# Optimization experiments

Hardware: AMD Instinct MI355X
Metric: run time of the kernel (lower is better)

## Reference

```python
import jax, jax.numpy as jnp
import numpy as np

B, S, H, L, V, T = 128, 512, 512, 2, 30, 64  # batch, enc len, hidden, layers, vocab, decode len


def _p(k, shape):
    return jax.random.normal(k, shape, jnp.float32) * 0.05


def setup_inputs() -> dict:
    key = jax.random.key(0)
    ks = jax.random.split(key, 24)
    inp = {"x": jax.random.normal(ks[0], (B, S, 2), jnp.float32)}
    inp["emb"] = _p(ks[1], (V, H))
    # encoder GRU (input dim 2 for layer 0, H for layer 1); PyTorch gate order r,z,n
    inp["enc_Wih0"] = _p(ks[2], (3 * H, 2));  inp["enc_Whh0"] = _p(ks[3], (3 * H, H))
    inp["enc_bih0"] = _p(ks[4], (3 * H,));    inp["enc_bhh0"] = _p(ks[5], (3 * H,))
    inp["enc_Wih1"] = _p(ks[6], (3 * H, H));  inp["enc_Whh1"] = _p(ks[7], (3 * H, H))
    inp["enc_bih1"] = _p(ks[8], (3 * H,));    inp["enc_bhh1"] = _p(ks[9], (3 * H,))
    # decoder GRU (input dim H)
    inp["dec_Wih0"] = _p(ks[10], (3 * H, H)); inp["dec_Whh0"] = _p(ks[11], (3 * H, H))
    inp["dec_bih0"] = _p(ks[12], (3 * H,));   inp["dec_bhh0"] = _p(ks[13], (3 * H,))
    inp["dec_Wih1"] = _p(ks[14], (3 * H, H)); inp["dec_Whh1"] = _p(ks[15], (3 * H, H))
    inp["dec_bih1"] = _p(ks[16], (3 * H,));   inp["dec_bhh1"] = _p(ks[17], (3 * H,))
    inp["fc_W"] = _p(ks[18], (V, 2 * H));     inp["fc_b"] = _p(ks[19], (V,))
    return inp


def gru_cell(xt, h, Wih, Whh, bih, bhh):
    gi = xt @ Wih.T + bih
    gh = h @ Whh.T + bhh
    i_r, i_z, i_n = jnp.split(gi, 3, axis=-1)
    h_r, h_z, h_n = jnp.split(gh, 3, axis=-1)
    r = jax.nn.sigmoid(i_r + h_r)
    z = jax.nn.sigmoid(i_z + h_z)
    n = jnp.tanh(i_n + r * h_n)
    return (1.0 - z) * n + z * h


def _forward(x, emb,
             enc_Wih0, enc_Whh0, enc_bih0, enc_bhh0,
             enc_Wih1, enc_Whh1, enc_bih1, enc_bhh1,
             dec_Wih0, dec_Whh0, dec_bih0, dec_bhh0,
             dec_Wih1, dec_Whh1, dec_bih1, dec_bhh1,
             fc_W, fc_b):
    b = x.shape[0]
    h0 = jnp.zeros((b, H), x.dtype)

    # ---- encoder: 2-layer GRU scanned over time ----
    def enc_step(hs, xt):
        a = gru_cell(xt, hs[0], enc_Wih0, enc_Whh0, enc_bih0, enc_bhh0)
        c = gru_cell(a, hs[1], enc_Wih1, enc_Whh1, enc_bih1, enc_bhh1)
        return (a, c), c

    (e0, e1), out_enc_t = jax.lax.scan(enc_step, (h0, h0), x.transpose(1, 0, 2))
    out_enc = out_enc_t.transpose(1, 0, 2)  # [B, S, H]

    def dec_step(carry, _):
        (d0, d1), tok = carry
        e = emb[tok]  # [B, H]
        n0 = gru_cell(e, d0, dec_Wih0, dec_Whh0, dec_bih0, dec_bhh0)
        n1 = gru_cell(n0, d1, dec_Wih1, dec_Whh1, dec_bih1, dec_bhh1)
        out_dec = n1  # [B, H]
        sim = jnp.einsum('bsh,bh->bs', out_enc, out_dec)  # [B, S]
        # faithful to nn.Softmax() implicit dim on 3-D [B,S,1] tensor -> dim=0 (batch)
        att_w = jax.nn.softmax(sim, axis=0)
        attention = jnp.einsum('bs,bsh->bh', att_w, out_enc)  # [B, H]
        logits = jnp.concatenate([out_dec, attention], axis=-1) @ fc_W.T + fc_b  # [B, V]
        tok_next = jnp.argmax(logits, axis=-1)
        return ((n0, n1), tok_next), logits

    tok0 = jnp.zeros((b,), jnp.int32)
    ((f0, f1), _), logits_t = jax.lax.scan(dec_step, ((e0, e1), tok0), None, length=T)
    vec_out = logits_t.transpose(1, 0, 2)  # [B, T, V]
    hidden = jnp.stack([f0, f1], axis=0)   # [n_layers, B, H]
    return vec_out, hidden


def reference(x, emb,
              enc_Wih0, enc_Whh0, enc_bih0, enc_bhh0,
              enc_Wih1, enc_Whh1, enc_bih1, enc_bhh1,
              dec_Wih0, dec_Whh0, dec_bih0, dec_bhh0,
              dec_Wih1, dec_Whh1, dec_bih1, dec_bhh1,
              fc_W, fc_b):
    return _forward(x, emb,
                    enc_Wih0, enc_Whh0, enc_bih0, enc_bhh0,
                    enc_Wih1, enc_Whh1, enc_bih1, enc_bhh1,
                    dec_Wih0, dec_Whh0, dec_bih0, dec_bhh0,
                    dec_Wih1, dec_Whh1, dec_bih1, dec_bhh1,
                    fc_W, fc_b)
```

## Files before the change

kernel.cpp:

```cpp
#include <hip/hip_runtime.h>
#include <math.h>

typedef short  s16x8 __attribute__((ext_vector_type(8)));
typedef float  f32x4 __attribute__((ext_vector_type(4)));
typedef unsigned short u16;

#define MFMA16(a, b, c) __builtin_amdgcn_mfma_f32_16x16x32_bf16((a), (b), (c), 0, 0, 0)

#define BB 128
#define SS 512
#define HH 512
#define VV 30
#define TT 64

__device__ __forceinline__ float b2f(u16 v) {
  union { unsigned int u; float f; } c; c.u = ((unsigned int)v) << 16; return c.f;
}
__device__ __forceinline__ u16 f2b(float f) {
  union { float f; unsigned int u; } c; c.f = f;
  unsigned int r = (c.u + 0x7FFFu + ((c.u >> 16) & 1u)) >> 16;
  return (u16)r;
}
__device__ __forceinline__ float sigm(float x) { return 1.f / (1.f + expf(-x)); }
__device__ __forceinline__ s16x8 ldf(const u16* p) { return *(const s16x8*)p; }


__device__ __forceinline__ void gru_dual(
    int bx,
    const u16* __restrict__ A1s, const int* __restrict__ gather,
    const u16* __restrict__ A2s,
    const u16* __restrict__ Wihs, const u16* __restrict__ Whhs,
    const float* __restrict__ bih, const float* __restrict__ bhh,
    float* __restrict__ hf, u16* __restrict__ hs_new,
    u16* __restrict__ oe, size_t oe_mstride)
{
  const int tid  = threadIdx.x;
  const int wave = tid >> 6, lane = tid & 63;
  const int lrow = lane & 15, lq = lane >> 4;
  const int j0 = (bx >> 1) * 16;
  const int m0 = (bx & 1) * 64 + wave * 16;

  const u16* a1p;
  if (gather) a1p = A1s + (size_t)gather[m0 + lrow] * 1024 + lq * 8;
  else        a1p = A1s + (size_t)(m0 + lrow) * 1024 + lq * 8;
  const u16* a2p = A2s + (size_t)(m0 + lrow) * 1024 + lq * 8;

  const u16* bp[6];
#pragma unroll
  for (int t = 0; t < 6; ++t) {
    int g = (t < 3) ? t : t - 3;
    const u16* W = (t < 3) ? Wihs : Whhs;
    bp[t] = W + (size_t)(g * HH + j0 + lrow) * 1024 + lq * 8;
  }

  f32x4 acc[6];
#pragma unroll
  for (int t = 0; t < 6; ++t) acc[t] = (f32x4){0.f, 0.f, 0.f, 0.f};

  for (int ks = 0; ks < HH; ks += 32) {
    s16x8 a1h = ldf(a1p), a1l = ldf(a1p + 512); a1p += 32;
    s16x8 a2h = ldf(a2p), a2l = ldf(a2p + 512); a2p += 32;
#pragma unroll
    for (int t = 0; t < 6; ++t) {
      s16x8 bh = ldf(bp[t]), bl = ldf(bp[t] + 512); bp[t] += 32;
      s16x8 ah = (t < 3) ? a1h : a2h;
      s16x8 al = (t < 3) ? a1l : a2l;
      acc[t] = MFMA16(ah, bh, acc[t]);
      acc[t] = MFMA16(ah, bl, acc[t]);
      acc[t] = MFMA16(al, bh, acc[t]);
    }
  }

  const int c = j0 + lrow;
  const float bir = bih[c], biz = bih[HH + c], bin = bih[2 * HH + c];
  const float bhr = bhh[c], bhz = bhh[HH + c], bhn = bhh[2 * HH + c];
#pragma unroll
  for (int r = 0; r < 4; ++r) {
    int m = m0 + lq * 4 + r;
    float ir = acc[0][r] + bir, iz = acc[1][r] + biz, inn = acc[2][r] + bin;
    float hr = acc[3][r] + bhr, hz = acc[4][r] + bhz, hn = acc[5][r] + bhn;
    float rr = sigm(ir + hr);
    float zz = sigm(iz + hz);
    float nn = tanhf(inn + rr * hn);
    float hp = hf[(size_t)m * HH + c];
    float hv = (1.f - zz) * nn + zz * hp;
    hf[(size_t)m * HH + c] = hv;
    u16 hi = f2b(hv);
    hs_new[(size_t)m * 1024 + c]       = hi;
    hs_new[(size_t)m * 1024 + 512 + c] = f2b(hv - b2f(hi));
    if (oe) oe[(size_t)m * oe_mstride + c] = hi;
  }
}

__device__ __forceinline__ void gru_l0(
    int bx, int p,
    const float* __restrict__ x, const float* __restrict__ Wih0,
    const u16* __restrict__ Whh0s,
    const float* __restrict__ bih0, const float* __restrict__ bhh0,
    const u16* __restrict__ As,
    float* __restrict__ af, u16* __restrict__ as_new)
{
  const int tid  = threadIdx.x;
  const int wave = tid >> 6, lane = tid & 63;
  const int lrow = lane & 15, lq = lane >> 4;
  const int j0 = bx * 16;
  const int mw = wave * 32;

  const u16* ap0 = As + (size_t)(mw + lrow) * 1024 + lq * 8;
  const u16* ap1 = As + (size_t)(mw + 16 + lrow) * 1024 + lq * 8;
  const u16* bp[3];
#pragma unroll
  for (int t = 0; t < 3; ++t)
    bp[t] = Whh0s + (size_t)(t * HH + j0 + lrow) * 1024 + lq * 8;

  f32x4 acc[2][3];
#pragma unroll
  for (int i = 0; i < 2; ++i)
#pragma unroll
    for (int t = 0; t < 3; ++t) acc[i][t] = (f32x4){0.f, 0.f, 0.f, 0.f};

  for (int ks = 0; ks < HH; ks += 32) {
    s16x8 a0h = ldf(ap0), a0l = ldf(ap0 + 512); ap0 += 32;
    s16x8 a1h = ldf(ap1), a1l = ldf(ap1 + 512); ap1 += 32;
#pragma unroll
    for (int t = 0; t < 3; ++t) {
      s16x8 bh = ldf(bp[t]), bl = ldf(bp[t] + 512); bp[t] += 32;
      acc[0][t] = MFMA16(a0h, bh, acc[0][t]);
      acc[0][t] = MFMA16(a0h, bl, acc[0][t]);
      acc[0][t] = MFMA16(a0l, bh, acc[0][t]);
      acc[1][t] = MFMA16(a1h, bh, acc[1][t]);
      acc[1][t] = MFMA16(a1h, bl, acc[1][t]);
      acc[1][t] = MFMA16(a1l, bh, acc[1][t]);
    }
  }

  const int c = j0 + lrow;
  const float bir = bih0[c], biz = bih0[HH + c], bin = bih0[2 * HH + c];
  const float bhr = bhh0[c], bhz = bhh0[HH + c], bhn = bhh0[2 * HH + c];
  const float wr0 = Wih0[(size_t)c * 2],            wr1 = Wih0[(size_t)c * 2 + 1];
  const float wz0 = Wih0[(size_t)(HH + c) * 2],     wz1 = Wih0[(size_t)(HH + c) * 2 + 1];
  const float wn0 = Wih0[(size_t)(2 * HH + c) * 2], wn1 = Wih0[(size_t)(2 * HH + c) * 2 + 1];
#pragma unroll
  for (int tm = 0; tm < 2; ++tm) {
#pragma unroll
    for (int r = 0; r < 4; ++r) {
      int m = mw + tm * 16 + lq * 4 + r;
      float x0 = x[((size_t)m * SS + p) * 2];
      float x1 = x[((size_t)m * SS + p) * 2 + 1];
      float ir  = bir + x0 * wr0 + x1 * wr1;
      float iz  = biz + x0 * wz0 + x1 * wz1;
      float inn = bin + x0 * wn0 + x1 * wn1;
      float hr = acc[tm][0][r] + bhr, hz = acc[tm][1][r] + bhz, hn = acc[tm][2][r] + bhn;
      float rr = sigm(ir + hr);
      float zz = sigm(iz + hz);
      float nn = tanhf(inn + rr * hn);
      float hp = af[(size_t)m * HH + c];
      float hv = (1.f - zz) * nn + zz * hp;
      af[(size_t)m * HH + c] = hv;
      u16 hi = f2b(hv);
      as_new[(size_t)m * 1024 + c]       = hi;
      as_new[(size_t)m * 1024 + 512 + c] = f2b(hv - b2f(hi));
    }
  }
}

__global__ __launch_bounds__(256) void enc_phase(
    int p,
    const float* __restrict__ x, const float* __restrict__ Wih0,
    const u16* __restrict__ Whh0s,
    const float* __restrict__ bih0, const float* __restrict__ bhh0,
    const u16* __restrict__ Wih1s, const u16* __restrict__ Whh1s,
    const float* __restrict__ bih1, const float* __restrict__ bhh1,
    const u16* abf_cur, u16* abf_new, float* af,
    const u16* cbf_cur, u16* cbf_new, float* cf,
    u16* out_enc)
{
  int bx = blockIdx.x;
  if (bx < 32) {
    if (p >= SS) return;
    gru_l0(bx, p, x, Wih0, Whh0s, bih0, bhh0, abf_cur, af, abf_new);
  } else {
    if (p == 0) return;
    u16* oe = out_enc + (size_t)(p - 1) * HH;
    gru_dual(bx - 32, abf_cur, nullptr, cbf_cur, Wih1s, Whh1s, bih1, bhh1,
             cf, cbf_new, oe, (size_t)SS * HH);
  }
}

__global__ __launch_bounds__(256) void dec_gru(
    const u16* A1s, const int* gather, const u16* A2s,
    const u16* __restrict__ Wihs, const u16* __restrict__ Whhs,
    const float* __restrict__ bih, const float* __restrict__ bhh,
    float* hf, u16* hs_new)
{
  gru_dual(blockIdx.x, A1s, gather, A2s, Wihs, Whhs, bih, bhh, hf, hs_new,
           nullptr, 0);
}

__global__ __launch_bounds__(256) void sim_kernel(
    const float* __restrict__ n1f, const u16* __restrict__ oe,
    float* __restrict__ simt)
{
  const int b = blockIdx.x >> 3, sc = blockIdx.x & 7;
  const int wave = threadIdx.x >> 6, lane = threadIdx.x & 63;
  float xr[8];
  const float* xp = n1f + (size_t)b * HH + lane * 8;
#pragma unroll
  for (int j = 0; j < 8; ++j) xr[j] = xp[j];
  int s0 = sc * 64 + wave * 16;
  for (int i = 0; i < 16; ++i) {
    int s = s0 + i;
    s16x8 ov = *(const s16x8*)(oe + ((size_t)b * SS + s) * HH + lane * 8);
    float acc = 0.f;
#pragma unroll
    for (int j = 0; j < 8; ++j) acc += xr[j] * b2f((u16)ov[j]);
    for (int off = 32; off; off >>= 1) acc += __shfl_down(acc, off);
    if (lane == 0) simt[(size_t)s * BB + b] = acc;
  }
}

__global__ __launch_bounds__(256) void attn_kernel(
    int tstep, const float* __restrict__ simt, const float* __restrict__ n1f,
    const u16* __restrict__ oe, const float* __restrict__ fcW,
    const float* __restrict__ fcb, float* __restrict__ dout,
    int* __restrict__ tok)
{
  __shared__ float wsm[SS];
  __shared__ float xv[2 * HH];
  __shared__ float lg[32];
  const int b = blockIdx.x, t = threadIdx.x;

  for (int s = t; s < SS; s += 256) {
    const float* row = simt + (size_t)s * BB;
    float mx = -1e30f;
    for (int i = 0; i < BB; ++i) mx = fmaxf(mx, row[i]);
    float e = 0.f;
    for (int i = 0; i < BB; ++i) e += expf(row[i] - mx);
    wsm[s] = expf(row[b] - mx) / e;
  }
  xv[t]       = n1f[(size_t)b * HH + t];
  xv[t + 256] = n1f[(size_t)b * HH + t + 256];
  __syncthreads();

  {
    float a0 = 0.f, a1 = 0.f;
    const u16* base = oe + (size_t)b * SS * HH;
    for (int s = 0; s < SS; ++s) {
      float w = wsm[s];
      a0 += w * b2f(base[(size_t)s * HH + t]);
      a1 += w * b2f(base[(size_t)s * HH + t + 256]);
    }
    xv[HH + t]       = a0;
    xv[HH + t + 256] = a1;
  }
  __syncthreads();

  int wave = t >> 6, lane = t & 63;
  for (int v = wave; v < VV; v += 4) {
    const float* wr = fcW + (size_t)v * (2 * HH);
    float acc = 0.f;
#pragma unroll
    for (int i = 0; i < 16; ++i) acc += xv[i * 64 + lane] * wr[i * 64 + lane];
    for (int off = 32; off; off >>= 1) acc += __shfl_down(acc, off);
    if (lane == 0) {
      float lv = acc + fcb[v];
      lg[v] = lv;
      dout[(size_t)b * (TT * VV) + (size_t)tstep * VV + v] = lv;
    }
  }
  __syncthreads();

  if (t == 0) {
    float best = lg[0]; int bi = 0;
    for (int v = 1; v < VV; ++v) if (lg[v] > best) { best = lg[v]; bi = v; }
    tok[b] = bi;
  }
}

__global__ __launch_bounds__(256) void splitk(
    const float* __restrict__ src, u16* __restrict__ dst, int n)
{
  int i = blockIdx.x * 256 + threadIdx.x;
  if (i >= n) return;
  int r = i >> 9, k = i & 511;
  float v = src[i];
  u16 hi = f2b(v);
  dst[(size_t)r * 1024 + k]       = hi;
  dst[(size_t)r * 1024 + 512 + k] = f2b(v - b2f(hi));
}

__global__ __launch_bounds__(256) void initk(
    float* af, float* cf, u16* b0, u16* b1, u16* b2, u16* b3, int* tok)
{
  int i = blockIdx.x * 256 + threadIdx.x;
  b0[i] = 0; b1[i] = 0; b2[i] = 0; b3[i] = 0;
  if (i < BB * HH) { af[i] = 0.f; cf[i] = 0.f; }
  if (i < BB) tok[i] = 0;
}

__global__ __launch_bounds__(256) void finalize(
    const float* __restrict__ d0, const float* __restrict__ d1,
    float* __restrict__ oh)
{
  int i = blockIdx.x * 256 + threadIdx.x;
  oh[i]           = d0[i];
  oh[BB * HH + i] = d1[i];
}

extern "C" void kernel_launch(void* const* d_in, const int* in_sizes, int n_in,
                              void* d_out, int out_size, void* d_ws, size_t ws_size,
                              hipStream_t stream) {
  const float* x     = (const float*)d_in[0];
  const float* emb   = (const float*)d_in[1];
  const float* eWih0 = (const float*)d_in[2];
  const float* eWhh0 = (const float*)d_in[3];
  const float* ebih0 = (const float*)d_in[4];
  const float* ebhh0 = (const float*)d_in[5];
  const float* eWih1 = (const float*)d_in[6];
  const float* eWhh1 = (const float*)d_in[7];
  const float* ebih1 = (const float*)d_in[8];
  const float* ebhh1 = (const float*)d_in[9];
  const float* dWih0 = (const float*)d_in[10];
  const float* dWhh0 = (const float*)d_in[11];
  const float* dbih0 = (const float*)d_in[12];
  const float* dbhh0 = (const float*)d_in[13];
  const float* dWih1 = (const float*)d_in[14];
  const float* dWhh1 = (const float*)d_in[15];
  const float* dbih1 = (const float*)d_in[16];
  const float* dbhh1 = (const float*)d_in[17];
  const float* fcW   = (const float*)d_in[18];
  const float* fcb   = (const float*)d_in[19];
  float* dout = (float*)d_out;

  char* wsb = (char*)d_ws;
  float* af   = (float*)(wsb + 0);
  float* cf   = (float*)(wsb + 262144);
  u16* ABF0   = (u16*)(wsb + 524288);
  u16* ABF1   = (u16*)(wsb + 786432);
  u16* CBF0   = (u16*)(wsb + 1048576);
  u16* CBF1   = (u16*)(wsb + 1310720);
  int* tok    = (int*)(wsb + 1572864);
  float* simt = (float*)(wsb + 1573376);
  u16* WeHH0  = (u16*)(wsb + 1835520);
  u16* WeIH1  = (u16*)(wsb + 4981248);
  u16* WeHH1  = (u16*)(wsb + 8126976);
  u16* WdIH0  = (u16*)(wsb + 11272704);
  u16* WdHH0  = (u16*)(wsb + 14418432);
  u16* WdIH1  = (u16*)(wsb + 17564160);
  u16* WdHH1  = (u16*)(wsb + 20709888);
  u16* EMBs   = (u16*)(wsb + 23855616);
  u16* oe     = (u16*)(wsb + 23917056);

  initk<<<512, 256, 0, stream>>>(af, cf, ABF0, ABF1, CBF0, CBF1, tok);

  const int WN = 3 * HH * HH;
  splitk<<<(WN + 255) / 256, 256, 0, stream>>>(eWhh0, WeHH0, WN);
  splitk<<<(WN + 255) / 256, 256, 0, stream>>>(eWih1, WeIH1, WN);
  splitk<<<(WN + 255) / 256, 256, 0, stream>>>(eWhh1, WeHH1, WN);
  splitk<<<(WN + 255) / 256, 256, 0, stream>>>(dWih0, WdIH0, WN);
  splitk<<<(WN + 255) / 256, 256, 0, stream>>>(dWhh0, WdHH0, WN);
  splitk<<<(WN + 255) / 256, 256, 0, stream>>>(dWih1, WdIH1, WN);
  splitk<<<(WN + 255) / 256, 256, 0, stream>>>(dWhh1, WdHH1, WN);
  splitk<<<(VV * HH + 255) / 256, 256, 0, stream>>>(emb, EMBs, VV * HH);

  const u16* pa = ABF0; u16* pa_n = ABF1;
  const u16* pc = CBF0; u16* pc_n = CBF1;
  for (int p = 0; p <= SS; ++p) {
    enc_phase<<<96, 256, 0, stream>>>(p, x, eWih0, WeHH0, ebih0, ebhh0,
                                      WeIH1, WeHH1, ebih1, ebhh1,
                                      pa, pa_n, af, pc, pc_n, cf, oe);
    const u16* tp;
    tp = pa; pa = pa_n; pa_n = (u16*)tp;
    tp = pc; pc = pc_n; pc_n = (u16*)tp;
  }
  const u16* d0c = ABF0; u16* d0n = ABF1;
  const u16* d1c = CBF1; u16* d1n = CBF0;

  for (int t = 0; t < TT; ++t) {
    dec_gru<<<64, 256, 0, stream>>>(EMBs, tok, d0c, WdIH0, WdHH0,
                                    dbih0, dbhh0, af, d0n);
    const u16* tp = d0c; d0c = d0n; d0n = (u16*)tp;
    dec_gru<<<64, 256, 0, stream>>>(d0c, nullptr, d1c, WdIH1, WdHH1,
                                    dbih1, dbhh1, cf, d1n);
    tp = d1c; d1c = d1n; d1n = (u16*)tp;
    sim_kernel<<<1024, 256, 0, stream>>>(cf, oe, simt);
    attn_kernel<<<128, 256, 0, stream>>>(t, simt, cf, oe, fcW, fcb, dout, tok);
  }

  finalize<<<256, 256, 0, stream>>>(af, cf, dout + (size_t)BB * TT * VV);
}
```

Measured before the change: 27.37 ms.

## Replace per-step kernel launches with cooperative persistent encoder and decoder kernels

The 513 encoder phase launches and the 256 decoder launches become two cooperative persistent kernels that step through time using grid-wide syncs. The eight weight split launches are merged into one kernel, and the similarity work is regrouped into 256 larger blocks. The aim is to remove per-launch overhead on these long sequential recurrences. In exchange, grid.sync barriers add latency per step, the decoder runs on only 256 blocks so parallelism in the sim phase drops, and non-cooperative fallback paths are kept in case the cooperative launch fails.

```diff
diff --git a/kernel.cpp b/kernel.cpp
--- a/kernel.cpp
+++ b/kernel.cpp
@@ -1,5 +1,8 @@
 #include <hip/hip_runtime.h>
+#include <hip/hip_cooperative_groups.h>
 #include <math.h>
+
+namespace cg = cooperative_groups;
 
 typedef short  s16x8 __attribute__((ext_vector_type(8)));
 typedef float  f32x4 __attribute__((ext_vector_type(4)));
@@ -164,6 +167,154 @@
   }
 }
 
+__device__ __forceinline__ void sim_block(
+    int bx, const float* __restrict__ n1f, const u16* __restrict__ oe,
+    float* __restrict__ simt)
+{
+  const int b = bx >> 1, sc = bx & 1;
+  const int wave = threadIdx.x >> 6, lane = threadIdx.x & 63;
+  float xr[8];
+  const float* xp = n1f + (size_t)b * HH + lane * 8;
+#pragma unroll
+  for (int j = 0; j < 8; ++j) xr[j] = xp[j];
+  int s0 = sc * 256 + wave * 64;
+  for (int i = 0; i < 64; ++i) {
+    int s = s0 + i;
+    s16x8 ov = *(const s16x8*)(oe + ((size_t)b * SS + s) * HH + lane * 8);
+    float acc = 0.f;
+#pragma unroll
+    for (int j = 0; j < 8; ++j) acc += xr[j] * b2f((u16)ov[j]);
+    for (int off = 32; off; off >>= 1) acc += __shfl_down(acc, off);
+    if (lane == 0) simt[(size_t)s * BB + b] = acc;
+  }
+}
+
+__device__ __forceinline__ void attn_block(
+    int b, int tstep, const float* __restrict__ simt, const float* __restrict__ n1f,
+    const u16* __restrict__ oe, const float* __restrict__ fcW,
+    const float* __restrict__ fcb, float* __restrict__ dout,
+    int* __restrict__ tok)
+{
+  __shared__ float wsm[SS];
+  __shared__ float xv[2 * HH];
+  __shared__ float lg[32];
+  const int t = threadIdx.x;
+
+  for (int s = t; s < SS; s += 256) {
+    const float* row = simt + (size_t)s * BB;
+    float mx = -1e30f;
+    for (int i = 0; i < BB; ++i) mx = fmaxf(mx, row[i]);
+    float e = 0.f;
+    for (int i = 0; i < BB; ++i) e += expf(row[i] - mx);
+    wsm[s] = expf(row[b] - mx) / e;
+  }
+  xv[t]       = n1f[(size_t)b * HH + t];
+  xv[t + 256] = n1f[(size_t)b * HH + t + 256];
+  __syncthreads();
+
+  {
+    float a0 = 0.f, a1 = 0.f;
+    const u16* base = oe + (size_t)b * SS * HH;
+    for (int s = 0; s < SS; ++s) {
+      float w = wsm[s];
+      a0 += w * b2f(base[(size_t)s * HH + t]);
+      a1 += w * b2f(base[(size_t)s * HH + t + 256]);
+    }
+    xv[HH + t]       = a0;
+    xv[HH + t + 256] = a1;
+  }
+  __syncthreads();
+
+  int wave = t >> 6, lane = t & 63;
+  for (int v = wave; v < VV; v += 4) {
+    const float* wr = fcW + (size_t)v * (2 * HH);
+    float acc = 0.f;
+#pragma unroll
+    for (int i = 0; i < 16; ++i) acc += xv[i * 64 + lane] * wr[i * 64 + lane];
+    for (int off = 32; off; off >>= 1) acc += __shfl_down(acc, off);
+    if (lane == 0) {
+      float lv = acc + fcb[v];
+      lg[v] = lv;
+      dout[(size_t)b * (TT * VV) + (size_t)tstep * VV + v] = lv;
+    }
+  }
+  __syncthreads();
+
+  if (t == 0) {
+    float best = lg[0]; int bi = 0;
+    for (int v = 1; v < VV; ++v) if (lg[v] > best) { best = lg[v]; bi = v; }
+    tok[b] = bi;
+  }
+}
+
+__global__ __launch_bounds__(256) void enc_persist(
+    const float* __restrict__ x, const float* __restrict__ Wih0,
+    const u16* __restrict__ Whh0s,
+    const float* __restrict__ bih0, const float* __restrict__ bhh0,
+    const u16* __restrict__ Wih1s, const u16* __restrict__ Whh1s,
+    const float* __restrict__ bih1, const float* __restrict__ bhh1,
+    u16* ABF0, u16* ABF1, float* af,
+    u16* CBF0, u16* CBF1, float* cf,
+    u16* out_enc)
+{
+  cg::grid_group grid = cg::this_grid();
+  const int bx = blockIdx.x;
+  const u16* pa = ABF0; u16* pa_n = ABF1;
+  const u16* pc = CBF0; u16* pc_n = CBF1;
+  for (int p = 0; p <= SS; ++p) {
+    if (bx < 32) {
+      if (p < SS) gru_l0(bx, p, x, Wih0, Whh0s, bih0, bhh0, pa, af, pa_n);
+    } else {
+      if (p > 0) {
+        u16* oe = out_enc + (size_t)(p - 1) * HH;
+        gru_dual(bx - 32, pa, nullptr, pc, Wih1s, Whh1s, bih1, bhh1,
+                 cf, pc_n, oe, (size_t)SS * HH);
+      }
+    }
+    grid.sync();
+    const u16* tp;
+    tp = pa; pa = pa_n; pa_n = (u16*)tp;
+    tp = pc; pc = pc_n; pc_n = (u16*)tp;
+  }
+}
+
+__global__ __launch_bounds__(256) void dec_persist(
+    const u16* __restrict__ EMBs, int* tok,
+    const u16* __restrict__ WdIH0, const u16* __restrict__ WdHH0,
+    const float* __restrict__ dbih0, const float* __restrict__ dbhh0,
+    const u16* __restrict__ WdIH1, const u16* __restrict__ WdHH1,
+    const float* __restrict__ dbih1, const float* __restrict__ dbhh1,
+    float* af, float* cf,
+    u16* D0A, u16* D0B, u16* D1A, u16* D1B,
+    const u16* __restrict__ oe, float* simt,
+    const float* __restrict__ fcW, const float* __restrict__ fcb,
+    float* dout)
+{
+  cg::grid_group grid = cg::this_grid();
+  const int bx = blockIdx.x;
+  const u16* d0c = D0A; u16* d0n = D0B;
+  const u16* d1c = D1A; u16* d1n = D1B;
+  for (int t = 0; t < TT; ++t) {
+    if (bx < 64)
+      gru_dual(bx, EMBs, tok, d0c, WdIH0, WdHH0, dbih0, dbhh0, af, d0n,
+               nullptr, 0);
+    grid.sync();
+    { const u16* tp = d0c; d0c = d0n; d0n = (u16*)tp; }
+
+    if (bx < 64)
+      gru_dual(bx, d0c, nullptr, d1c, WdIH1, WdHH1, dbih1, dbhh1, cf, d1n,
+               nullptr, 0);
+    grid.sync();
+    { const u16* tp = d1c; d1c = d1n; d1n = (u16*)tp; }
+
+    sim_block(bx, cf, oe, simt);
+    grid.sync();
+
+    if (bx < BB) attn_block(bx, t, simt, cf, oe, fcW, fcb, dout, tok);
+    grid.sync();
+  }
+}
+
 __global__ __launch_bounds__(256) void enc_phase(
     int p,
     const float* __restrict__ x, const float* __restrict__ Wih0,
@@ -201,22 +352,7 @@
     const float* __restrict__ n1f, const u16* __restrict__ oe,
     float* __restrict__ simt)
 {
-  const int b = blockIdx.x >> 3, sc = blockIdx.x & 7;
-  const int wave = threadIdx.x >> 6, lane = threadIdx.x & 63;
-  float xr[8];
-  const float* xp = n1f + (size_t)b * HH + lane * 8;
-#pragma unroll
-  for (int j = 0; j < 8; ++j) xr[j] = xp[j];
-  int s0 = sc * 64 + wave * 16;
-  for (int i = 0; i < 16; ++i) {
-    int s = s0 + i;
-    s16x8 ov = *(const s16x8*)(oe + ((size_t)b * SS + s) * HH + lane * 8);
-    float acc = 0.f;
-#pragma unroll
-    for (int j = 0; j < 8; ++j) acc += xr[j] * b2f((u16)ov[j]);
-    for (int off = 32; off; off >>= 1) acc += __shfl_down(acc, off);
-    if (lane == 0) simt[(size_t)s * BB + b] = acc;
-  }
+  sim_block(blockIdx.x, n1f, oe, simt);
 }
 
 __global__ __launch_bounds__(256) void attn_kernel(
@@ -225,68 +361,31 @@
     const float* __restrict__ fcb, float* __restrict__ dout,
     int* __restrict__ tok)
 {
-  __shared__ float wsm[SS];
-  __shared__ float xv[2 * HH];
-  __shared__ float lg[32];
-  const int b = blockIdx.x, t = threadIdx.x;
-
-  for (int s = t; s < SS; s += 256) {
-    const float* row = simt + (size_t)s * BB;
-    float mx = -1e30f;
-    for (int i = 0; i < BB; ++i) mx = fmaxf(mx, row[i]);
-    float e = 0.f;
-    for (int i = 0; i < BB; ++i) e += expf(row[i] - mx);
-    wsm[s] = expf(row[b] - mx) / e;
-  }
-  xv[t]       = n1f[(size_t)b * HH + t];
-  xv[t + 256] = n1f[(size_t)b * HH + t + 256];
-  __syncthreads();
-
-  {
-    float a0 = 0.f, a1 = 0.f;
-    const u16* base = oe + (size_t)b * SS * HH;
-    for (int s = 0; s < SS; ++s) {
-      float w = wsm[s];
-      a0 += w * b2f(base[(size_t)s * HH + t]);
-      a1 += w * b2f(base[(size_t)s * HH + t + 256]);
-    }
-    xv[HH + t]       = a0;
-    xv[HH + t + 256] = a1;
-  }
-  __syncthreads();
-
-  int wave = t >> 6, lane = t & 63;
-  for (int v = wave; v < VV; v += 4) {
-    const float* wr = fcW + (size_t)v * (2 * HH);
-    float acc = 0.f;
-#pragma unroll
-    for (int i = 0; i < 16; ++i) acc += xv[i * 64 + lane] * wr[i * 64 + lane];
-    for (int off = 32; off; off >>= 1) acc += __shfl_down(acc, off);
-    if (lane == 0) {
-      float lv = acc + fcb[v];
-      lg[v] = lv;
-      dout[(size_t)b * (TT * VV) + (size_t)tstep * VV + v] = lv;
-    }
-  }
-  __syncthreads();
-
-  if (t == 0) {
-    float best = lg[0]; int bi = 0;
-    for (int v = 1; v < VV; ++v) if (lg[v] > best) { best = lg[v]; bi = v; }
-    tok[b] = bi;
-  }
-}
-
-__global__ __launch_bounds__(256) void splitk(
-    const float* __restrict__ src, u16* __restrict__ dst, int n)
-{
+  attn_block(blockIdx.x, tstep, simt, n1f, oe, fcW, fcb, dout, tok);
+}
+
+__global__ __launch_bounds__(256) void splitall(
+    const float* __restrict__ s0, u16* d0, const float* __restrict__ s1, u16* d1,
+    const float* __restrict__ s2, u16* d2, const float* __restrict__ s3, u16* d3,
+    const float* __restrict__ s4, u16* d4, const float* __restrict__ s5, u16* d5,
+    const float* __restrict__ s6, u16* d6, const float* __restrict__ s7, u16* d7)
+{
+  const int WN = 3 * HH * HH;
   int i = blockIdx.x * 256 + threadIdx.x;
-  if (i >= n) return;
-  int r = i >> 9, k = i & 511;
-  float v = src[i];
+  const float* s; u16* d; int j;
+  if      (i < 1 * WN) { s = s0; d = d0; j = i; }
+  else if (i < 2 * WN) { s = s1; d = d1; j = i - 1 * WN; }
+  else if (i < 3 * WN) { s = s2; d = d2; j = i - 2 * WN; }
+  else if (i < 4 * WN) { s = s3; d = d3; j = i - 3 * WN; }
+  else if (i < 5 * WN) { s = s4; d = d4; j = i - 4 * WN; }
+  else if (i < 6 * WN) { s = s5; d = d5; j = i - 5 * WN; }
+  else if (i < 7 * WN) { s = s6; d = d6; j = i - 6 * WN; }
+  else { j = i - 7 * WN; if (j >= VV * HH) return; s = s7; d = d7; }
+  int r = j >> 9, k = j & 511;
+  float v = s[j];
   u16 hi = f2b(v);
-  dst[(size_t)r * 1024 + k]       = hi;
-  dst[(size_t)r * 1024 + 512 + k] = f2b(v - b2f(hi));
+  d[(size_t)r * 1024 + k]       = hi;
+  d[(size_t)r * 1024 + 512 + k] = f2b(v - b2f(hi));
 }
 
 __global__ __launch_bounds__(256) void initk(
@@ -353,38 +452,59 @@
 
   initk<<<512, 256, 0, stream>>>(af, cf, ABF0, ABF1, CBF0, CBF1, tok);
 
-  const int WN = 3 * HH * HH;
-  splitk<<<(WN + 255) / 256, 256, 0, stream>>>(eWhh0, WeHH0, WN);
-  splitk<<<(WN + 255) / 256, 256, 0, stream>>>(eWih1, WeIH1, WN);
-  splitk<<<(WN + 255) / 256, 256, 0, stream>>>(eWhh1, WeHH1, WN);
-  splitk<<<(WN + 255) / 256, 256, 0, stream>>>(dWih0, WdIH0, WN);
-  splitk<<<(WN + 255) / 256, 256, 0, stream>>>(dWhh0, WdHH0, WN);
-  splitk<<<(WN + 255) / 256, 256, 0, stream>>>(dWih1, WdIH1, WN);
-  splitk<<<(WN + 255) / 256, 256, 0, stream>>>(dWhh1, WdHH1, WN);
-  splitk<<<(VV * HH + 255) / 256, 256, 0, stream>>>(emb, EMBs, VV * HH);
-
-  const u16* pa = ABF0; u16* pa_n = ABF1;
-  const u16* pc = CBF0; u16* pc_n = CBF1;
-  for (int p = 0; p <= SS; ++p) {
-    enc_phase<<<96, 256, 0, stream>>>(p, x, eWih0, WeHH0, ebih0, ebhh0,
-                                      WeIH1, WeHH1, ebih1, ebhh1,
-                                      pa, pa_n, af, pc, pc_n, cf, oe);
-    const u16* tp;
-    tp = pa; pa = pa_n; pa_n = (u16*)tp;
-    tp = pc; pc = pc_n; pc_n = (u16*)tp;
-  }
-  const u16* d0c = ABF0; u16* d0n = ABF1;
-  const u16* d1c = CBF1; u16* d1n = CBF0;
-
-  for (int t = 0; t < TT; ++t) {
-    dec_gru<<<64, 256, 0, stream>>>(EMBs, tok, d0c, WdIH0, WdHH0,
-                                    dbih0, dbhh0, af, d0n);
-    const u16* tp = d0c; d0c = d0n; d0n = (u16*)tp;
-    dec_gru<<<64, 256, 0, stream>>>(d0c, nullptr, d1c, WdIH1, WdHH1,
-                                    dbih1, dbhh1, cf, d1n);
-    tp = d1c; d1c = d1n; d1n = (u16*)tp;
-    sim_kernel<<<1024, 256, 0, stream>>>(cf, oe, simt);
-    attn_kernel<<<128, 256, 0, stream>>>(t, simt, cf, oe, fcW, fcb, dout, tok);
+  splitall<<<21564, 256, 0, stream>>>(eWhh0, WeHH0, eWih1, WeIH1, eWhh1, WeHH1,
+                                      dWih0, WdIH0, dWhh0, WdHH0, dWih1, WdIH1,
+                                      dWhh1, WdHH1, emb, EMBs);
+
+  {
+    void* ea[] = {
+      (void*)&x, (void*)&eWih0, (void*)&WeHH0, (void*)&ebih0, (void*)&ebhh0,
+      (void*)&WeIH1, (void*)&WeHH1, (void*)&ebih1, (void*)&ebhh1,
+      (void*)&ABF0, (void*)&ABF1, (void*)&af,
+      (void*)&CBF0, (void*)&CBF1, (void*)&cf, (void*)&oe
+    };
+    hipError_t e = hipLaunchCooperativeKernel((void*)enc_persist, dim3(96),
+                                              dim3(256), ea, 0, stream);
+    if (e != hipSuccess) {
+      const u16* pa = ABF0; u16* pa_n = ABF1;
+      const u16* pc = CBF0; u16* pc_n = CBF1;
+      for (int p = 0; p <= SS; ++p) {
+        enc_phase<<<96, 256, 0, stream>>>(p, x, eWih0, WeHH0, ebih0, ebhh0,
+                                          WeIH1, WeHH1, ebih1, ebhh1,
+                                          pa, pa_n, af, pc, pc_n, cf, oe);
+        const u16* tp;
+        tp = pa; pa = pa_n; pa_n = (u16*)tp;
+        tp = pc; pc = pc_n; pc_n = (u16*)tp;
+      }
+    }
+  }
+
+  {
+    u16* D0A = ABF0; u16* D0B = ABF1; u16* D1A = CBF1; u16* D1B = CBF0;
+    void* da[] = {
+      (void*)&EMBs, (void*)&tok,
+      (void*)&WdIH0, (void*)&WdHH0, (void*)&dbih0, (void*)&dbhh0,
+      (void*)&WdIH1, (void*)&WdHH1, (void*)&dbih1, (void*)&dbhh1,
+      (void*)&af, (void*)&cf,
+      (void*)&D0A, (void*)&D0B, (void*)&D1A, (void*)&D1B,
+      (void*)&oe, (void*)&simt, (void*)&fcW, (void*)&fcb, (void*)&dout
+    };
+    hipError_t e = hipLaunchCooperativeKernel((void*)dec_persist, dim3(256),
+                                              dim3(256), da, 0, stream);
+    if (e != hipSuccess) {
+      const u16* d0c = D0A; u16* d0n = D0B;
+      const u16* d1c = D1A; u16* d1n = D1B;
+      for (int t = 0; t < TT; ++t) {
+        dec_gru<<<64, 256, 0, stream>>>(EMBs, tok, d0c, WdIH0, WdHH0,
+                                        dbih0, dbhh0, af, d0n);
+        const u16* tp = d0c; d0c = d0n; d0n = (u16*)tp;
+        dec_gru<<<64, 256, 0, stream>>>(d0c, nullptr, d1c, WdIH1, WdHH1,
+                                        dbih1, dbhh1, cf, d1n);
+        tp = d1c; d1c = d1n; d1n = (u16*)tp;
+        sim_kernel<<<256, 256, 0, stream>>>(cf, oe, simt);
+        attn_kernel<<<128, 256, 0, stream>>>(t, simt, cf, oe, fcW, fcb, dout, tok);
+      }
+    }
   }
 
   finalize<<<256, 256, 0, stream>>>(af, cf, dout + (size_t)BB * TT * VV);
```

Result: slower. 40.54 ms (+48.1%).
